# Kernel optimization log

Hardware: AMD Instinct MI355X
Metric: run time of the kernel (lower is better)

The kernel has to match this reference:

```python
import jax, jax.numpy as jnp
import numpy as np

H = 16  # num_heads

def setup_inputs() -> dict:
    key = jax.random.key(0)
    ks = jax.random.split(key, 5)
    C = 1024
    x = jax.random.normal(ks[0], (4, 2048, C), dtype=jnp.float32)
    # torch nn.Linear params: weight (out, in), bias (out,)
    qkv_w = jax.random.normal(ks[1], (3 * C, C), dtype=jnp.float32) * (C ** -0.5)
    qkv_b = jnp.zeros((3 * C,), dtype=jnp.float32)
    proj_w = jax.random.normal(ks[2], (C, C), dtype=jnp.float32) * (C ** -0.5)
    proj_b = jnp.zeros((C,), dtype=jnp.float32)
    return {"x": x, "qkv_w": qkv_w, "qkv_b": qkv_b, "proj_w": proj_w, "proj_b": proj_b}

def reference(x, qkv_w, qkv_b, proj_w, proj_b):
    B, T, C = x.shape
    hd = C // H
    scale = hd ** -0.5
    qkv = x @ qkv_w.T + qkv_b                      # [B,T,3C]
    qkv = qkv.reshape(B, T, 3, H, hd)
    q, k, v = jnp.moveaxis(qkv, 2, 0)              # each [B,T,H,hd]
    q = q.transpose(0, 2, 1, 3)                    # [B,H,T,hd]
    k = k.transpose(0, 2, 1, 3)
    v = v.transpose(0, 2, 1, 3)
    attn = jnp.einsum('bhqd,bhkd->bhqk', q, k) * scale
    attn = jax.nn.softmax(attn, axis=-1)           # dropout is identity at eval
    out = jnp.einsum('bhqk,bhkd->bhqd', attn, v)   # [B,H,T,hd]
    out = out.transpose(0, 2, 1, 3).reshape(B, T, C)
    return out @ proj_w.T + proj_b
```

## Files before the change

kernel.cpp:

```cpp
#include <hip/hip_runtime.h>


typedef _Float16 f16x8 __attribute__((ext_vector_type(8)));
typedef _Float16 f16x4 __attribute__((ext_vector_type(4)));
typedef float f32x4 __attribute__((ext_vector_type(4)));

__device__ __forceinline__ uint4 cvt8h(const float* p) {
    float4 a = *(const float4*)p, b = *(const float4*)(p + 4);
    union { _Float16 h[8]; uint4 u; } t;
    t.h[0] = (_Float16)a.x; t.h[1] = (_Float16)a.y;
    t.h[2] = (_Float16)a.z; t.h[3] = (_Float16)a.w;
    t.h[4] = (_Float16)b.x; t.h[5] = (_Float16)b.y;
    t.h[6] = (_Float16)b.z; t.h[7] = (_Float16)b.w;
    return t.u;
}

__device__ __forceinline__ void dma16(const _Float16* g, _Float16* l) {
    __builtin_amdgcn_global_load_lds(
        (const __attribute__((address_space(1))) unsigned int*)g,
        (__attribute__((address_space(3))) unsigned int*)l, 16, 0, 0);
}

__global__ __launch_bounds__(256) void cvt_fp16(
    const float* __restrict__ x, const float* __restrict__ w1,
    const float* __restrict__ w2,
    _Float16* __restrict__ xh, _Float16* __restrict__ w1h,
    _Float16* __restrict__ w2h)
{
    const int g = blockIdx.x * 256 + threadIdx.x;
    const float* src; _Float16* dst; int off;
    if (g < 1048576)      { src = x;  dst = xh;  off = g; }
    else if (g < 1441792) { src = w1; dst = w1h; off = g - 1048576; }
    else                  { src = w2; dst = w2h; off = g - 1441792; }
    const size_t e = (size_t)off * 8;
    *(uint4*)(dst + e) = cvt8h(src + e);
}

__global__ __launch_bounds__(256) void qkv_gemm(
    const _Float16* __restrict__ X, const _Float16* __restrict__ W,
    const float* __restrict__ Bias,
    _Float16* __restrict__ qws, _Float16* __restrict__ kws,
    _Float16* __restrict__ vtws)
{
    __shared__ _Float16 sA[128 * 32];
    __shared__ _Float16 sB[128 * 32];
    const int tid = threadIdx.x;
    const int wave = tid >> 6, lane = tid & 63;
    const int wm = (wave >> 1) * 64, wn = (wave & 1) * 64;
    const int lr = lane & 15, lq = lane >> 4;
    const int m0 = blockIdx.y * 128, n0 = blockIdx.x * 128;
    const int s = n0 >> 10;

    const int drow = wave * 16 + (lane >> 2);
    const int dcol = (lane & 3) * 8;
    _Float16* ldsA = sA + wave * 512;
    _Float16* ldsB = sB + wave * 512;
    const _Float16* gA = X + (size_t)(m0 + drow) * 1024 + dcol;
    const _Float16* gB = W + (size_t)(n0 + drow) * 1024 + dcol;

    f32x4 acc[4][4] = {};

    for (int k0 = 0; k0 < 1024; k0 += 32) {
        dma16(gA + k0, ldsA);
        dma16(gA + (size_t)64 * 1024 + k0, ldsA + 2048);
        dma16(gB + k0, ldsB);
        dma16(gB + (size_t)64 * 1024 + k0, ldsB + 2048);
        __syncthreads();
        f16x8 af[4], bf[4];
        #pragma unroll
        for (int i = 0; i < 4; ++i) {
            af[i] = *(const f16x8*)&sA[(wm + i * 16 + lr) * 32 + lq * 8];
            bf[i] = *(const f16x8*)&sB[(wn + i * 16 + lr) * 32 + lq * 8];
        }
        #pragma unroll
        for (int mi = 0; mi < 4; ++mi)
            #pragma unroll
            for (int ni = 0; ni < 4; ++ni)
                acc[mi][ni] = __builtin_amdgcn_mfma_f32_16x16x32_f16(
                    af[mi], bf[ni], acc[mi][ni], 0, 0, 0);
        __syncthreads();
    }

    #pragma unroll
    for (int mi = 0; mi < 4; ++mi) {
        #pragma unroll
        for (int ni = 0; ni < 4; ++ni) {
            const int n = n0 + wn + ni * 16 + lr;
            const float bv = Bias[n];
            const int h = (n >> 6) & 15, d = n & 63;
            const int mbase = m0 + wm + mi * 16 + lq * 4;
            const int b = mbase >> 11, t0 = mbase & 2047;
            const int bh = b * 16 + h;
            if (s == 0) {
                #pragma unroll
                for (int r = 0; r < 4; ++r)
                    qws[((size_t)bh * 2048 + t0 + r) * 64 + d] =
                        (_Float16)((acc[mi][ni][r] + bv) * 0.18033688f);
            } else if (s == 1) {
                #pragma unroll
                for (int r = 0; r < 4; ++r)
                    kws[((size_t)bh * 2048 + t0 + r) * 64 + d] =
                        (_Float16)(acc[mi][ni][r] + bv);
            } else {
                f16x4 pk;
                #pragma unroll
                for (int r = 0; r < 4; ++r) pk[r] = (_Float16)(acc[mi][ni][r] + bv);
                *(f16x4*)&vtws[((size_t)bh * 64 + d) * 2048 + t0] = pk;
            }
        }
    }
}

__global__ __launch_bounds__(256, 4) void attn_kernel(
    const _Float16* __restrict__ qws,
    const _Float16* __restrict__ kws,
    const _Float16* __restrict__ vtws,
    _Float16* __restrict__ ows)
{
    __shared__ _Float16 sP[4][32][72];
    __shared__ _Float16 sK[64][72];
    __shared__ _Float16 sV[64][72];
    const int bid = blockIdx.x;
    const int bh = (bid & 7) * 8 + ((bid >> 3) & 7);
    const int qb = bid >> 6;
    const int tid = threadIdx.x, wave = tid >> 6, lane = tid & 63;
    const int lr = lane & 15, lq = lane >> 4;

    _Float16* sQ = &sP[0][0][0];
    {
        const _Float16* gq = qws + ((size_t)bh * 2048 + qb * 128) * 64;
        for (int i = tid; i < 1024; i += 256)
            *(uint4*)&sQ[i * 8] = *(const uint4*)&gq[i * 8];
    }
    __syncthreads();
    f16x8 aQ[2][2];
    #pragma unroll
    for (int mb = 0; mb < 2; ++mb)
        #pragma unroll
        for (int ks = 0; ks < 2; ++ks)
            aQ[mb][ks] = *(const f16x8*)&sQ[(wave * 32 + mb * 16 + lr) * 64 + ks * 32 + lq * 8];

    f32x4 o[2][4] = {};
    float l_loc[2] = {};

    for (int kt = 0; kt < 32; ++kt) {
        const _Float16* gk = kws + ((size_t)bh * 2048 + kt * 64) * 64;
        const _Float16* gv = vtws + (size_t)bh * 64 * 2048 + kt * 64;
        __syncthreads();
        for (int i = tid; i < 512; i += 256) {
            const int row = i >> 3, c = (i & 7) * 8;
            *(uint4*)&sK[row][c] = *(const uint4*)&gk[row * 64 + c];
            *(uint4*)&sV[row][c] = *(const uint4*)&gv[(size_t)row * 2048 + c];
        }
        __syncthreads();

        f16x8 bK[2][4];
        #pragma unroll
        for (int ks = 0; ks < 2; ++ks)
            #pragma unroll
            for (int nb = 0; nb < 4; ++nb)
                bK[ks][nb] = *(const f16x8*)&sK[nb * 16 + lr][ks * 32 + lq * 8];
        f32x4 st[4][2] = {};
        #pragma unroll
        for (int nb = 0; nb < 4; ++nb)
            #pragma unroll
            for (int mb = 0; mb < 2; ++mb) {
                st[nb][mb] = __builtin_amdgcn_mfma_f32_16x16x32_f16(
                    bK[0][nb], aQ[mb][0], st[nb][mb], 0, 0, 0);
                st[nb][mb] = __builtin_amdgcn_mfma_f32_16x16x32_f16(
                    bK[1][nb], aQ[mb][1], st[nb][mb], 0, 0, 0);
            }

        #pragma unroll
        for (int nb = 0; nb < 4; ++nb)
            #pragma unroll
            for (int mb = 0; mb < 2; ++mb) {
                f16x4 pk;
                #pragma unroll
                for (int reg = 0; reg < 4; ++reg) {
                    const float p = exp2f(st[nb][mb][reg]);
                    l_loc[mb] += p;
                    pk[reg] = (_Float16)p;
                }
                *(f16x4*)&sP[wave][mb * 16 + lr][nb * 16 + lq * 4] = pk;
            }

        f16x8 vA[2][4], pB[2][2];
        #pragma unroll
        for (int ks = 0; ks < 2; ++ks)
            #pragma unroll
            for (int db = 0; db < 4; ++db)
                vA[ks][db] = *(const f16x8*)&sV[db * 16 + lr][ks * 32 + lq * 8];
        #pragma unroll
        for (int mb = 0; mb < 2; ++mb)
            #pragma unroll
            for (int ks = 0; ks < 2; ++ks)
                pB[mb][ks] = *(const f16x8*)&sP[wave][mb * 16 + lr][ks * 32 + lq * 8];
        #pragma unroll
        for (int mb = 0; mb < 2; ++mb)
            #pragma unroll
            for (int db = 0; db < 4; ++db) {
                o[mb][db] = __builtin_amdgcn_mfma_f32_16x16x32_f16(
                    vA[0][db], pB[mb][0], o[mb][db], 0, 0, 0);
                o[mb][db] = __builtin_amdgcn_mfma_f32_16x16x32_f16(
                    vA[1][db], pB[mb][1], o[mb][db], 0, 0, 0);
            }
    }

    const int b = bh >> 4, h = bh & 15;
    #pragma unroll
    for (int mb = 0; mb < 2; ++mb) {
        float l = l_loc[mb];
        l += __shfl_xor(l, 16, 64);
        l += __shfl_xor(l, 32, 64);
        const float linv = 1.0f / l;
        const int t = qb * 128 + wave * 32 + mb * 16 + lr;
        #pragma unroll
        for (int db = 0; db < 4; ++db) {
            f16x4 pk;
            #pragma unroll
            for (int reg = 0; reg < 4; ++reg)
                pk[reg] = (_Float16)(o[mb][db][reg] * linv);
            *(f16x4*)&ows[((size_t)(b * 2048 + t)) * 1024 + h * 64 + db * 16 + lq * 4] = pk;
        }
    }
}

__global__ __launch_bounds__(256) void proj_gemm(
    const _Float16* __restrict__ A, const _Float16* __restrict__ W,
    const float* __restrict__ Bias, float* __restrict__ out)
{
    __shared__ _Float16 sA[128 * 32];
    __shared__ _Float16 sB[128 * 32];
    const int tid = threadIdx.x;
    const int wave = tid >> 6, lane = tid & 63;
    const int wm = (wave >> 1) * 64, wn = (wave & 1) * 64;
    const int lr = lane & 15, lq = lane >> 4;
    const int m0 = blockIdx.y * 128, n0 = blockIdx.x * 128;

    const int drow = wave * 16 + (lane >> 2);
    const int dcol = (lane & 3) * 8;
    _Float16* ldsA = sA + wave * 512;
    _Float16* ldsB = sB + wave * 512;
    const _Float16* gA = A + (size_t)(m0 + drow) * 1024 + dcol;
    const _Float16* gB = W + (size_t)(n0 + drow) * 1024 + dcol;

    f32x4 acc[4][4] = {};

    for (int k0 = 0; k0 < 1024; k0 += 32) {
        dma16(gA + k0, ldsA);
        dma16(gA + (size_t)64 * 1024 + k0, ldsA + 2048);
        dma16(gB + k0, ldsB);
        dma16(gB + (size_t)64 * 1024 + k0, ldsB + 2048);
        __syncthreads();
        f16x8 af[4], bf[4];
        #pragma unroll
        for (int i = 0; i < 4; ++i) {
            af[i] = *(const f16x8*)&sA[(wm + i * 16 + lr) * 32 + lq * 8];
            bf[i] = *(const f16x8*)&sB[(wn + i * 16 + lr) * 32 + lq * 8];
        }
        #pragma unroll
        for (int mi = 0; mi < 4; ++mi)
            #pragma unroll
            for (int ni = 0; ni < 4; ++ni)
                acc[mi][ni] = __builtin_amdgcn_mfma_f32_16x16x32_f16(
                    af[mi], bf[ni], acc[mi][ni], 0, 0, 0);
        __syncthreads();
    }

    #pragma unroll
    for (int mi = 0; mi < 4; ++mi) {
        #pragma unroll
        for (int ni = 0; ni < 4; ++ni) {
            const int n = n0 + wn + ni * 16 + lr;
            const float bv = Bias[n];
            #pragma unroll
            for (int r = 0; r < 4; ++r) {
                const int m = m0 + wm + mi * 16 + lq * 4 + r;
                out[(size_t)m * 1024 + n] = acc[mi][ni][r] + bv;
            }
        }
    }
}

extern "C" void kernel_launch(void* const* d_in, const int* in_sizes, int n_in,
                              void* d_out, int out_size, void* d_ws, size_t ws_size,
                              hipStream_t stream) {
    const float* x      = (const float*)d_in[0];
    const float* qkv_w  = (const float*)d_in[1];
    const float* qkv_b  = (const float*)d_in[2];
    const float* proj_w = (const float*)d_in[3];
    const float* proj_b = (const float*)d_in[4];
    float* out = (float*)d_out;

    char* ws = (char*)d_ws;
    _Float16* qws  = (_Float16*)(ws);
    _Float16* kws  = (_Float16*)(ws + 16777216u);
    _Float16* vtws = (_Float16*)(ws + 33554432u);
    _Float16* ows  = (_Float16*)(ws + 50331648u);
    _Float16* Xh   = (_Float16*)(ws + 67108864u);
    _Float16* Wqh  = (_Float16*)(ws + 83886080u);
    _Float16* Wph  = (_Float16*)(ws + 90177536u);

    cvt_fp16<<<dim3(6144), 256, 0, stream>>>(x, qkv_w, proj_w, Xh, Wqh, Wph);
    qkv_gemm<<<dim3(24, 64), 256, 0, stream>>>(Xh, Wqh, qkv_b, qws, kws, vtws);
    attn_kernel<<<dim3(1024), 256, 0, stream>>>(qws, kws, vtws, ows);
    proj_gemm<<<dim3(8, 64), 256, 0, stream>>>(ows, Wph, proj_b, out);
}
```

Before: 299.7 us.

## Double-buffer K/V tiles with async LDS DMA and swizzled layout in attention

Replaces the synchronous per-tile K/V copy through registers with global_load_lds DMA into double-buffered shared memory. The next tile is prefetched while the current one is computed, which is meant to hide global memory latency. The shared layout now uses an XOR swizzle instead of padding to avoid LDS bank conflicts. Q is read straight from global memory rather than staged through LDS, and s_setprio brackets the MFMA blocks. The risk is that the DMA completion wait at the end-of-loop barrier may be insufficient, and the swizzle index math must exactly match the reads.

```diff
diff --git a/kernel.cpp b/kernel.cpp
--- a/kernel.cpp
+++ b/kernel.cpp
@@ -117,50 +117,64 @@
     const _Float16* __restrict__ vtws,
     _Float16* __restrict__ ows)
 {
+    __shared__ _Float16 sK[2][64][64];
+    __shared__ _Float16 sV[2][64][64];
     __shared__ _Float16 sP[4][32][72];
-    __shared__ _Float16 sK[64][72];
-    __shared__ _Float16 sV[64][72];
     const int bid = blockIdx.x;
     const int bh = (bid & 7) * 8 + ((bid >> 3) & 7);
     const int qb = bid >> 6;
     const int tid = threadIdx.x, wave = tid >> 6, lane = tid & 63;
     const int lr = lane & 15, lq = lane >> 4;
 
-    _Float16* sQ = &sP[0][0][0];
-    {
-        const _Float16* gq = qws + ((size_t)bh * 2048 + qb * 128) * 64;
-        for (int i = tid; i < 1024; i += 256)
-            *(uint4*)&sQ[i * 8] = *(const uint4*)&gq[i * 8];
-    }
-    __syncthreads();
+    const _Float16* gq = qws + ((size_t)bh * 2048 + qb * 128) * 64;
     f16x8 aQ[2][2];
     #pragma unroll
     for (int mb = 0; mb < 2; ++mb)
         #pragma unroll
         for (int ks = 0; ks < 2; ++ks)
-            aQ[mb][ks] = *(const f16x8*)&sQ[(wave * 32 + mb * 16 + lr) * 64 + ks * 32 + lq * 8];
+            aQ[mb][ks] = *(const f16x8*)&gq[(wave * 32 + mb * 16 + lr) * 64 + ks * 32 + lq * 8];
+
+    const int l8 = lane >> 3;
+    const int swzcol = (((lane & 7) * 16) ^ (l8 << 4)) >> 1;
+    const int krow = wave * 8 + l8;
+    const _Float16* gkbase = kws + (size_t)bh * 2048 * 64 + krow * 64 + swzcol;
+    const _Float16* gvbase = vtws + (size_t)bh * 64 * 2048 + (size_t)krow * 2048 + swzcol;
+    _Float16* dK0 = &sK[0][0][0] + wave * 512;
+    _Float16* dV0 = &sV[0][0][0] + wave * 512;
+
+    dma16(gkbase,                      dK0);
+    dma16(gkbase + 32 * 64,            dK0 + 2048);
+    dma16(gvbase,                      dV0);
+    dma16(gvbase + (size_t)32 * 2048,  dV0 + 2048);
+    __syncthreads();
+
+    const int cidx0 = ((lq * 16) ^ ((lr & 7) << 4)) >> 1;
+    const int cidx1 = ((64 + lq * 16) ^ ((lr & 7) << 4)) >> 1;
 
     f32x4 o[2][4] = {};
     float l_loc[2] = {};
 
     for (int kt = 0; kt < 32; ++kt) {
-        const _Float16* gk = kws + ((size_t)bh * 2048 + kt * 64) * 64;
-        const _Float16* gv = vtws + (size_t)bh * 64 * 2048 + kt * 64;
-        __syncthreads();
-        for (int i = tid; i < 512; i += 256) {
-            const int row = i >> 3, c = (i & 7) * 8;
-            *(uint4*)&sK[row][c] = *(const uint4*)&gk[row * 64 + c];
-            *(uint4*)&sV[row][c] = *(const uint4*)&gv[(size_t)row * 2048 + c];
-        }
-        __syncthreads();
+        const int cur = kt & 1, nxt = cur ^ 1;
+        if (kt < 31) {
+            const _Float16* gk = gkbase + (size_t)(kt + 1) * 4096;
+            const _Float16* gv = gvbase + (kt + 1) * 64;
+            _Float16* dK = &sK[nxt][0][0] + wave * 512;
+            _Float16* dV = &sV[nxt][0][0] + wave * 512;
+            dma16(gk,                     dK);
+            dma16(gk + 32 * 64,           dK + 2048);
+            dma16(gv,                     dV);
+            dma16(gv + (size_t)32 * 2048, dV + 2048);
+        }
 
         f16x8 bK[2][4];
         #pragma unroll
-        for (int ks = 0; ks < 2; ++ks)
-            #pragma unroll
-            for (int nb = 0; nb < 4; ++nb)
-                bK[ks][nb] = *(const f16x8*)&sK[nb * 16 + lr][ks * 32 + lq * 8];
+        for (int nb = 0; nb < 4; ++nb) {
+            bK[0][nb] = *(const f16x8*)&sK[cur][nb * 16 + lr][cidx0];
+            bK[1][nb] = *(const f16x8*)&sK[cur][nb * 16 + lr][cidx1];
+        }
         f32x4 st[4][2] = {};
+        __builtin_amdgcn_s_setprio(1);
         #pragma unroll
         for (int nb = 0; nb < 4; ++nb)
             #pragma unroll
@@ -170,6 +184,7 @@
                 st[nb][mb] = __builtin_amdgcn_mfma_f32_16x16x32_f16(
                     bK[1][nb], aQ[mb][1], st[nb][mb], 0, 0, 0);
             }
+        __builtin_amdgcn_s_setprio(0);
 
         #pragma unroll
         for (int nb = 0; nb < 4; ++nb)
@@ -187,15 +202,16 @@
 
         f16x8 vA[2][4], pB[2][2];
         #pragma unroll
-        for (int ks = 0; ks < 2; ++ks)
-            #pragma unroll
-            for (int db = 0; db < 4; ++db)
-                vA[ks][db] = *(const f16x8*)&sV[db * 16 + lr][ks * 32 + lq * 8];
+        for (int db = 0; db < 4; ++db) {
+            vA[0][db] = *(const f16x8*)&sV[cur][db * 16 + lr][cidx0];
+            vA[1][db] = *(const f16x8*)&sV[cur][db * 16 + lr][cidx1];
+        }
         #pragma unroll
         for (int mb = 0; mb < 2; ++mb)
             #pragma unroll
             for (int ks = 0; ks < 2; ++ks)
                 pB[mb][ks] = *(const f16x8*)&sP[wave][mb * 16 + lr][ks * 32 + lq * 8];
+        __builtin_amdgcn_s_setprio(1);
         #pragma unroll
         for (int mb = 0; mb < 2; ++mb)
             #pragma unroll
@@ -205,6 +221,9 @@
                 o[mb][db] = __builtin_amdgcn_mfma_f32_16x16x32_f16(
                     vA[1][db], pB[mb][1], o[mb][db], 0, 0, 0);
             }
+        __builtin_amdgcn_s_setprio(0);
+
+        __syncthreads();
     }
 
     const int b = bh >> 4, h = bh & 15;
```

After: 310.7 us. 1.04x slower.

## Keep softmax probabilities in registers and feed PV via 16x16x16 MFMA

Applied to the files above, without the earlier changes.

The P tile no longer goes through LDS. The QK^T accumulator layout is reused directly as the B operand of 16x16x16 f16 MFMAs, with packed RTZ conversion, and V fragments are read per 16-key slice. This removes the LDS write and read of P and frees LDS by loading Q straight from global memory into registers. It also wraps the MFMA sections in s_setprio. The trade-off is twice as many MFMA instructions at half the K depth, plus round-toward-zero conversion of the probabilities.

```diff
diff --git a/kernel.cpp b/kernel.cpp
--- a/kernel.cpp
+++ b/kernel.cpp
@@ -3,6 +3,7 @@
 
 typedef _Float16 f16x8 __attribute__((ext_vector_type(8)));
 typedef _Float16 f16x4 __attribute__((ext_vector_type(4)));
+typedef __fp16 h16x2 __attribute__((ext_vector_type(2)));
 typedef float f32x4 __attribute__((ext_vector_type(4)));
 
 __device__ __forceinline__ uint4 cvt8h(const float* p) {
@@ -117,7 +118,6 @@
     const _Float16* __restrict__ vtws,
     _Float16* __restrict__ ows)
 {
-    __shared__ _Float16 sP[4][32][72];
     __shared__ _Float16 sK[64][72];
     __shared__ _Float16 sV[64][72];
     const int bid = blockIdx.x;
@@ -126,19 +126,13 @@
     const int tid = threadIdx.x, wave = tid >> 6, lane = tid & 63;
     const int lr = lane & 15, lq = lane >> 4;
 
-    _Float16* sQ = &sP[0][0][0];
-    {
-        const _Float16* gq = qws + ((size_t)bh * 2048 + qb * 128) * 64;
-        for (int i = tid; i < 1024; i += 256)
-            *(uint4*)&sQ[i * 8] = *(const uint4*)&gq[i * 8];
-    }
-    __syncthreads();
+    const _Float16* gq = qws + ((size_t)bh * 2048 + qb * 128) * 64;
     f16x8 aQ[2][2];
     #pragma unroll
     for (int mb = 0; mb < 2; ++mb)
         #pragma unroll
         for (int ks = 0; ks < 2; ++ks)
-            aQ[mb][ks] = *(const f16x8*)&sQ[(wave * 32 + mb * 16 + lr) * 64 + ks * 32 + lq * 8];
+            aQ[mb][ks] = *(const f16x8*)&gq[(wave * 32 + mb * 16 + lr) * 64 + ks * 32 + lq * 8];
 
     f32x4 o[2][4] = {};
     float l_loc[2] = {};
@@ -161,6 +155,7 @@
             for (int nb = 0; nb < 4; ++nb)
                 bK[ks][nb] = *(const f16x8*)&sK[nb * 16 + lr][ks * 32 + lq * 8];
         f32x4 st[4][2] = {};
+        __builtin_amdgcn_s_setprio(1);
         #pragma unroll
         for (int nb = 0; nb < 4; ++nb)
             #pragma unroll
@@ -170,41 +165,39 @@
                 st[nb][mb] = __builtin_amdgcn_mfma_f32_16x16x32_f16(
                     bK[1][nb], aQ[mb][1], st[nb][mb], 0, 0, 0);
             }
-
+        __builtin_amdgcn_s_setprio(0);
+
+        f16x4 pB16[4][2];
         #pragma unroll
         for (int nb = 0; nb < 4; ++nb)
             #pragma unroll
             for (int mb = 0; mb < 2; ++mb) {
-                f16x4 pk;
+                float e0 = exp2f(st[nb][mb][0]);
+                float e1 = exp2f(st[nb][mb][1]);
+                float e2 = exp2f(st[nb][mb][2]);
+                float e3 = exp2f(st[nb][mb][3]);
+                l_loc[mb] += (e0 + e1) + (e2 + e3);
+                union { h16x2 v2[2]; f16x4 v4; } u;
+                u.v2[0] = __builtin_amdgcn_cvt_pkrtz(e0, e1);
+                u.v2[1] = __builtin_amdgcn_cvt_pkrtz(e2, e3);
+                pB16[nb][mb] = u.v4;
+            }
+
+        __builtin_amdgcn_s_setprio(1);
+        #pragma unroll
+        for (int nb = 0; nb < 4; ++nb) {
+            f16x4 vA16[4];
+            #pragma unroll
+            for (int db = 0; db < 4; ++db)
+                vA16[db] = *(const f16x4*)&sV[db * 16 + lr][nb * 16 + lq * 4];
+            #pragma unroll
+            for (int mb = 0; mb < 2; ++mb)
                 #pragma unroll
-                for (int reg = 0; reg < 4; ++reg) {
-                    const float p = exp2f(st[nb][mb][reg]);
-                    l_loc[mb] += p;
-                    pk[reg] = (_Float16)p;
-                }
-                *(f16x4*)&sP[wave][mb * 16 + lr][nb * 16 + lq * 4] = pk;
-            }
-
-        f16x8 vA[2][4], pB[2][2];
-        #pragma unroll
-        for (int ks = 0; ks < 2; ++ks)
-            #pragma unroll
-            for (int db = 0; db < 4; ++db)
-                vA[ks][db] = *(const f16x8*)&sV[db * 16 + lr][ks * 32 + lq * 8];
-        #pragma unroll
-        for (int mb = 0; mb < 2; ++mb)
-            #pragma unroll
-            for (int ks = 0; ks < 2; ++ks)
-                pB[mb][ks] = *(const f16x8*)&sP[wave][mb * 16 + lr][ks * 32 + lq * 8];
-        #pragma unroll
-        for (int mb = 0; mb < 2; ++mb)
-            #pragma unroll
-            for (int db = 0; db < 4; ++db) {
-                o[mb][db] = __builtin_amdgcn_mfma_f32_16x16x32_f16(
-                    vA[0][db], pB[mb][0], o[mb][db], 0, 0, 0);
-                o[mb][db] = __builtin_amdgcn_mfma_f32_16x16x32_f16(
-                    vA[1][db], pB[mb][1], o[mb][db], 0, 0, 0);
-            }
+                for (int db = 0; db < 4; ++db)
+                    o[mb][db] = __builtin_amdgcn_mfma_f32_16x16x16f16(
+                        vA16[db], pB16[nb][mb], o[mb][db], 0, 0, 0);
+        }
+        __builtin_amdgcn_s_setprio(0);
     }
 
     const int b = bh >> 4, h = bh & 15;
```

New measurement: 306.5 us. 1.02x slower.
